# Performance work log

Measured on AMD Instinct MI355X. Metric: run time of the kernel, lower is better.

## Reference

```python
import jax, jax.numpy as jnp
import numpy as np

K = 1024       # vq_codebook_size
DC = 64        # vq_code_dim
BETA = 0.25    # commitment cost
DECAY = 0.99   # EMA decay
EPS = 1e-05


def setup_inputs() -> dict:
    key = jax.random.key(0)
    k1, k2, k3 = jax.random.split(key, 3)
    B, H, W = 32, 64, 64
    return {
        "z_e": jax.random.normal(k1, (B, DC, H, W), dtype=jnp.float32),
        "embedding": jax.random.normal(k2, (K, DC), dtype=jnp.float32),
        "cluster_size": jnp.ones((K,), dtype=jnp.float32),
        "embed_avg": jax.random.normal(k3, (K, DC), dtype=jnp.float32),
    }


def reference(z_e, embedding, cluster_size, embed_avg):
    B, D, H, W = z_e.shape
    # flat: [N, D] detached codes, N = B*H*W
    flat = jax.lax.stop_gradient(z_e).transpose(0, 2, 3, 1).reshape(-1, D).astype(jnp.float32)
    distances = ((flat ** 2).sum(1, keepdims=True)
                 + (embedding ** 2).sum(1)
                 - 2.0 * flat @ embedding.T)
    indices = jnp.argmin(distances, axis=-1)          # [N]
    z_q_flat = embedding[indices]                      # gather [N, D]

    # EMA statistics (training path): one-hot sums via segment_sum (scatter-add)
    counts = jax.ops.segment_sum(jnp.ones_like(indices, dtype=jnp.float32), indices, num_segments=K)
    dw = jax.ops.segment_sum(flat, indices, num_segments=K)  # encodings.T @ flat
    new_cluster_size = cluster_size * DECAY + (1.0 - DECAY) * counts
    new_embed_avg = embed_avg * DECAY + (1.0 - DECAY) * dw
    n = new_cluster_size.sum()
    smoothed = (new_cluster_size + EPS) / (n + K * EPS) * n
    new_embedding = new_embed_avg / smoothed[:, None]

    z_q = z_q_flat.reshape(B, H, W, D).transpose(0, 3, 1, 2)  # [B, D, H, W]
    commitment_loss = BETA * jnp.mean((z_e.astype(jnp.float32) - jax.lax.stop_gradient(z_q)) ** 2)
    # straight-through estimator
    z_q_st = z_e + jax.lax.stop_gradient(z_q.astype(z_e.dtype) - z_e)
    return (z_q_st, indices.reshape(B, H, W), commitment_loss,
            new_embedding, new_cluster_size, new_embed_avg)
```

## Files before the change

kernel.cpp:

```cpp
#include <hip/hip_runtime.h>

#define KCB   1024
#define DCV   64
#define HWN   4096
#define CHW   262144
#define NTOT  131072

#define O_ZQ   0
#define O_IDX  8388608
#define O_LOSS 8519680
#define O_NE   8519681
#define O_NCS  8585217
#define O_NEA  8586241

#define W_LOSS  0
#define W_CTR   64
#define W_E2    256
#define W_SM    4352
#define W_HIT   8448
#define W_LOT   139520
#define W_EMBT  270592
#define W_RLIST 532736

#define RCAP   65536
#define MARGIN 0.015f

typedef __attribute__((ext_vector_type(8))) short short8v;
typedef __attribute__((ext_vector_type(4))) float f32x4;

__device__ __forceinline__ unsigned short rne16(float f) {
    unsigned u = __float_as_uint(f);
    unsigned r = (u + 0x7FFFu + ((u >> 16) & 1u)) >> 16;
    return (unsigned short)r;
}

__global__ __launch_bounds__(256) void k_init(
    const float* __restrict__ emb, const float* __restrict__ ea,
    const float* __restrict__ cs, float* __restrict__ out,
    float* __restrict__ e2, short* __restrict__ hiT, short* __restrict__ loT,
    float* __restrict__ embT, double* __restrict__ loss, int* __restrict__ ctr)
{
    int j = blockIdx.x * 256 + threadIdx.x;
    out[O_NEA + j] = 0.99f * ea[j];

    {
        int code = j >> 6, d = j & 63;
        embT[d * KCB + code] = emb[j];
    }
    if (j < KCB) {
        out[O_NCS + j] = 0.99f * cs[j];
        const float* er = emb + j * DCV;
        float s = 0.f;
        #pragma unroll
        for (int d = 0; d < DCV; ++d) { float v = er[d]; s = fmaf(v, v, s); }
        e2[j] = s;
    }
    if (j < 8192) {
        int code = j >> 3, q = j & 7;
        const float* src = emb + code * DCV + q * 8;
        short8v h, l;
        #pragma unroll
        for (int t = 0; t < 8; ++t) {
            float x = src[t];
            unsigned short hb = rne16(x);
            float xh = __uint_as_float(((unsigned)hb) << 16);
            h[t] = (short)hb;
            l[t] = (short)rne16(x - xh);
        }
        *(short8v*)(hiT + (size_t)(q * KCB + code) * 8) = h;
        *(short8v*)(loT + (size_t)(q * KCB + code) * 8) = l;
    }
    if (j == 0) { *loss = 0.0; *ctr = 0; }
}

__global__ __launch_bounds__(256, 4) void k_dist(
    const float* __restrict__ ze, const short* __restrict__ hiT,
    const short* __restrict__ loT, const float* __restrict__ e2g,
    float* __restrict__ out, int* __restrict__ ctr, int* __restrict__ rlist)
{
    __shared__ short ldsH[8 * 128 * 8];
    __shared__ short ldsL[8 * 128 * 8];
    __shared__ float e2s[KCB];

    int tid  = threadIdx.x;
    int lane = tid & 63, w = tid >> 6;
    int g = lane >> 4, c = lane & 15;

    for (int i = tid; i < KCB; i += 256) e2s[i] = e2g[i];

    int rowbase = blockIdx.x * 128 + w * 32;
    short8v ahi[2][2], alo[2][2];
    #pragma unroll
    for (int t = 0; t < 2; ++t) {
        int n = rowbase + t * 16 + c;
        const float* base = ze + (size_t)(n >> 12) * CHW + (n & 4095);
        #pragma unroll
        for (int kh = 0; kh < 2; ++kh) {
            #pragma unroll
            for (int j = 0; j < 8; ++j) {
                int k = kh * 32 + g * 8 + j;
                float x = base[(size_t)k * HWN];
                unsigned short hb = rne16(x);
                float xh = __uint_as_float(((unsigned)hb) << 16);
                ahi[t][kh][j] = (short)hb;
                alo[t][kh][j] = (short)rne16(x - xh);
            }
        }
    }

    float best[8], second[8];
    int   bidx[8];
    #pragma unroll
    for (int i = 0; i < 8; ++i) { best[i] = 3.4e38f; second[i] = 3.4e38f; bidx[i] = 0; }

    for (int ch = 0; ch < 8; ++ch) {
        __syncthreads();
        #pragma unroll
        for (int r = 0; r < 8; ++r) {
            int u = r * 256 + tid;
            int arr = u >> 10;
            int rest = u & 1023;
            int q = rest >> 7, lc = rest & 127;
            const short* s = (arr ? loT : hiT) + (size_t)(q * KCB + ch * 128 + lc) * 8;
            short* d = (arr ? ldsL : ldsH) + rest * 8;
            *(short8v*)d = *(const short8v*)s;
        }
        __syncthreads();

        #pragma unroll 1
        for (int sub = 0; sub < 8; ++sub) {
            int boff = (sub * 16 + c) * 8;
            short8v bh0 = *(const short8v*)&ldsH[(g * 128) * 8 + boff];
            short8v bh1 = *(const short8v*)&ldsH[((4 + g) * 128) * 8 + boff];
            short8v bl0 = *(const short8v*)&ldsL[(g * 128) * 8 + boff];
            short8v bl1 = *(const short8v*)&ldsL[((4 + g) * 128) * 8 + boff];

            f32x4 a0 = {0.f, 0.f, 0.f, 0.f}, a1 = {0.f, 0.f, 0.f, 0.f};
            a0 = __builtin_amdgcn_mfma_f32_16x16x32_bf16(ahi[0][0], bh0, a0, 0, 0, 0);
            a1 = __builtin_amdgcn_mfma_f32_16x16x32_bf16(ahi[1][0], bh0, a1, 0, 0, 0);
            a0 = __builtin_amdgcn_mfma_f32_16x16x32_bf16(ahi[0][1], bh1, a0, 0, 0, 0);
            a1 = __builtin_amdgcn_mfma_f32_16x16x32_bf16(ahi[1][1], bh1, a1, 0, 0, 0);
            a0 = __builtin_amdgcn_mfma_f32_16x16x32_bf16(ahi[0][0], bl0, a0, 0, 0, 0);
            a1 = __builtin_amdgcn_mfma_f32_16x16x32_bf16(ahi[1][0], bl0, a1, 0, 0, 0);
            a0 = __builtin_amdgcn_mfma_f32_16x16x32_bf16(ahi[0][1], bl1, a0, 0, 0, 0);
            a1 = __builtin_amdgcn_mfma_f32_16x16x32_bf16(ahi[1][1], bl1, a1, 0, 0, 0);
            a0 = __builtin_amdgcn_mfma_f32_16x16x32_bf16(alo[0][0], bh0, a0, 0, 0, 0);
            a1 = __builtin_amdgcn_mfma_f32_16x16x32_bf16(alo[1][0], bh0, a1, 0, 0, 0);
            a0 = __builtin_amdgcn_mfma_f32_16x16x32_bf16(alo[0][1], bh1, a0, 0, 0, 0);
            a1 = __builtin_amdgcn_mfma_f32_16x16x32_bf16(alo[1][1], bh1, a1, 0, 0, 0);

            float e2v = e2s[ch * 128 + sub * 16 + c];
            int  code = ch * 128 + sub * 16 + c;
            #pragma unroll
            for (int t = 0; t < 2; ++t) {
                f32x4 av = t ? a1 : a0;
                #pragma unroll
                for (int r = 0; r < 4; ++r) {
                    int i = t * 4 + r;
                    float s = fmaf(-2.f, av[r], e2v);
                    bool lb = s < best[i];
                    float m = lb ? best[i] : s;
                    second[i] = fminf(second[i], m);
                    best[i]   = fminf(best[i], s);
                    bidx[i]   = lb ? code : bidx[i];
                }
            }
        }
    }

    #pragma unroll
    for (int i = 0; i < 8; ++i) {
        float b = best[i], s2 = second[i];
        int bi = bidx[i];
        #pragma unroll
        for (int m = 1; m < 16; m <<= 1) {
            float ob = __shfl_xor(b, m, 64);
            float os = __shfl_xor(s2, m, 64);
            int   oi = __shfl_xor(bi, m, 64);
            float ns = fminf(fmaxf(b, ob), fminf(s2, os));
            bi = (ob < b || (ob == b && oi < bi)) ? oi : bi;
            b  = fminf(b, ob);
            s2 = ns;
        }
        if (c == 0) {
            int t = i >> 2, r = i & 3;
            int n = rowbase + t * 16 + g * 4 + r;
            out[O_IDX + n] = (float)bi;
            if (s2 - b < MARGIN) {
                int p = atomicAdd(ctr, 1);
                if (p < RCAP) rlist[p] = n;
            }
        }
    }
}

__global__ __launch_bounds__(256) void k_refine(
    const float* __restrict__ ze, const float* __restrict__ emb,
    float* __restrict__ out, const int* __restrict__ ctr,
    const int* __restrict__ rlist)
{
    int lane = threadIdx.x & 63;
    int gw   = (blockIdx.x * blockDim.x + threadIdx.x) >> 6;
    int nw   = (gridDim.x * blockDim.x) >> 6;
    int cnt  = *ctr;
    if (cnt > RCAP) cnt = RCAP;

    for (int i = gw; i < cnt; i += nw) {
        int n = rlist[i];
        const float* zp = ze + (size_t)(n >> 12) * CHW + (n & 4095);
        float x[DCV];
        #pragma unroll
        for (int d = 0; d < DCV; ++d) x[d] = zp[(size_t)d * HWN];

        double bd = 1e300;
        int    bi = 0;
        #pragma unroll 1
        for (int cc = 0; cc < KCB / 64; ++cc) {
            int k = cc * 64 + lane;
            const float4* eb4 = (const float4*)(emb + k * DCV);
            double a0 = 0.0, a1 = 0.0;
            #pragma unroll
            for (int q = 0; q < DCV / 4; ++q) {
                float4 v = eb4[q];
                double d0 = (double)x[q * 4 + 0] - (double)v.x;
                double d1 = (double)x[q * 4 + 1] - (double)v.y;
                double d2 = (double)x[q * 4 + 2] - (double)v.z;
                double d3 = (double)x[q * 4 + 3] - (double)v.w;
                a0 = fma(d0, d0, a0); a1 = fma(d1, d1, a1);
                a0 = fma(d2, d2, a0); a1 = fma(d3, d3, a1);
            }
            double dist = a0 + a1;
            if (dist < bd || (dist == bd && k < bi)) { bd = dist; bi = k; }
        }
        #pragma unroll
        for (int off = 32; off > 0; off >>= 1) {
            double od = __shfl_xor(bd, off, 64);
            int    oi = __shfl_xor(bi, off, 64);
            if (od < bd || (od == bd && oi < bi)) { bd = od; bi = oi; }
        }
        if (lane == 0) out[O_IDX + n] = (float)bi;
    }
}

__global__ __launch_bounds__(256) void k_final(
    const float* __restrict__ ze, const float* __restrict__ embT,
    float* __restrict__ out, double* __restrict__ loss)
{
    int blk = blockIdx.x;
    int b   = blk >> 4;
    int hw  = (blk & 15) * 256 + threadIdx.x;
    int n   = b * HWN + hw;

    int myidx = (int)out[O_IDX + n];

    const float* zp = ze  + (size_t)b * CHW + hw;
    float*       zq = out + O_ZQ + (size_t)b * CHW + hw;

    float lp = 0.f;
    #pragma unroll 8
    for (int d = 0; d < DCV; ++d) {
        float x = zp[(size_t)d * HWN];
        float e = embT[d * KCB + myidx];
        float df = x - e;
        lp = fmaf(df, df, lp);
        zq[(size_t)d * HWN] = x + (e - x);
    }

    #pragma unroll
    for (int off = 32; off > 0; off >>= 1) lp += __shfl_down(lp, off, 64);

    __shared__ float wsum[4];
    int lane = threadIdx.x & 63, wid = threadIdx.x >> 6;
    if (lane == 0) wsum[wid] = lp;
    __syncthreads();
    if (threadIdx.x == 0) {
        double s = (double)wsum[0] + wsum[1] + wsum[2] + wsum[3];
        atomicAdd(loss, s);
    }
}

__global__ __launch_bounds__(256) void k_dw_part(
    const float* __restrict__ ze, const float* __restrict__ outIdx,
    float* __restrict__ out)
{
    int gidx = blockIdx.x >> 5, b = blockIdx.x & 31;
    __shared__ float acc[8 * KCB];
    __shared__ float cnt[KCB];
    for (int i = threadIdx.x; i < 8 * KCB; i += 256) acc[i] = 0.f;
    if (gidx == 0) for (int i = threadIdx.x; i < KCB; i += 256) cnt[i] = 0.f;
    __syncthreads();

    const float* zp  = ze + (size_t)b * CHW + (size_t)gidx * 8 * HWN;
    const float* ipf = outIdx + b * HWN;
    for (int hw = threadIdx.x; hw < HWN; hw += 256) {
        int idx = (int)ipf[hw];
        #pragma unroll
        for (int i = 0; i < 8; ++i) atomicAdd(&acc[idx * 8 + i], zp[(size_t)i * HWN + hw]);
        if (gidx == 0) atomicAdd(&cnt[idx], 1.f);
    }
    __syncthreads();

    for (int j = threadIdx.x; j < 8192; j += 256) {
        float v = acc[j];
        if (v != 0.f) atomicAdd(&out[O_NEA + (j >> 3) * DCV + gidx * 8 + (j & 7)], 0.01f * v);
    }
    if (gidx == 0)
        for (int k = threadIdx.x; k < KCB; k += 256) {
            float cv = cnt[k];
            if (cv != 0.f) atomicAdd(&out[O_NCS + k], 0.01f * cv);
        }
}

__global__ __launch_bounds__(1024) void k_stats(
    float* __restrict__ out, float* __restrict__ sm,
    const double* __restrict__ loss)
{
    int k = threadIdx.x;
    float ncs = out[O_NCS + k];
    __shared__ float red[KCB];
    red[k] = ncs;
    __syncthreads();
    for (int s = 512; s > 0; s >>= 1) {
        if (k < s) red[k] += red[k + s];
        __syncthreads();
    }
    float n = red[0];
    sm[k] = (ncs + 1e-5f) / (n + (float)KCB * 1e-5f) * n;
    if (k == 0) out[O_LOSS] = (float)(0.25 * (*loss) / (double)(NTOT * DCV));
}

__global__ __launch_bounds__(256) void k_embed(
    float* __restrict__ out, const float* __restrict__ sm)
{
    int j = blockIdx.x * 256 + threadIdx.x;
    out[O_NE + j] = out[O_NEA + j] / sm[j >> 6];
}

extern "C" void kernel_launch(void* const* d_in, const int* in_sizes, int n_in,
                              void* d_out, int out_size, void* d_ws, size_t ws_size,
                              hipStream_t stream)
{
    const float* ze  = (const float*)d_in[0];
    const float* emb = (const float*)d_in[1];
    const float* cs  = (const float*)d_in[2];
    const float* ea  = (const float*)d_in[3];
    float* out = (float*)d_out;

    char*   w     = (char*)d_ws;
    double* loss  = (double*)(w + W_LOSS);
    int*    ctr   = (int*)(w + W_CTR);
    float*  e2    = (float*)(w + W_E2);
    float*  sm    = (float*)(w + W_SM);
    short*  hiT   = (short*)(w + W_HIT);
    short*  loT   = (short*)(w + W_LOT);
    float*  embT  = (float*)(w + W_EMBT);
    int*    rlist = (int*)(w + W_RLIST);

    k_init   <<<256, 256, 0, stream>>>(emb, ea, cs, out, e2, hiT, loT, embT, loss, ctr);
    k_dist   <<<1024, 256, 0, stream>>>(ze, hiT, loT, e2, out, ctr, rlist);
    k_refine <<<256, 256, 0, stream>>>(ze, emb, out, ctr, rlist);
    k_final  <<<512, 256, 0, stream>>>(ze, embT, out, loss);
    k_dw_part<<<256, 256, 0, stream>>>(ze, (const float*)(out + O_IDX), out);
    k_stats  <<<1, 1024, 0, stream>>>(out, sm, loss);
    k_embed  <<<256, 256, 0, stream>>>(out, sm);
}
```

Before: 268.9 us.

## Fuse z_q/loss pass with dw scatter, merge stats into embed, tune dist

Merges the straight-through/commitment-loss pass into the per-batch dw/count scatter kernel so z_e and the indices are read once, and folds the cluster-size reduction and embedding normalisation into a single kernel. Seven launches become five. It also lowers the refine margin for ambiguous argmin candidates and relaxes the occupancy hint on the distance kernel. The fused kernel runs only 256 blocks, fewer than the separate 512-block z_q pass, which may lower memory parallelism. The smaller margin risks missing near-tie rows that need exact refinement.

```diff
diff --git a/kernel.cpp b/kernel.cpp
--- a/kernel.cpp
+++ b/kernel.cpp
@@ -16,14 +16,13 @@
 #define W_LOSS  0
 #define W_CTR   64
 #define W_E2    256
-#define W_SM    4352
 #define W_HIT   8448
 #define W_LOT   139520
 #define W_EMBT  270592
 #define W_RLIST 532736
 
 #define RCAP   65536
-#define MARGIN 0.015f
+#define MARGIN 0.01f
 
 typedef __attribute__((ext_vector_type(8))) short short8v;
 typedef __attribute__((ext_vector_type(4))) float f32x4;
@@ -73,7 +72,7 @@
     if (j == 0) { *loss = 0.0; *ctr = 0; }
 }
 
-__global__ __launch_bounds__(256, 4) void k_dist(
+__global__ __launch_bounds__(256, 2) void k_dist(
     const float* __restrict__ ze, const short* __restrict__ hiT,
     const short* __restrict__ loT, const float* __restrict__ e2g,
     float* __restrict__ out, int* __restrict__ ctr, int* __restrict__ rlist)
@@ -242,34 +241,40 @@
     }
 }
 
-__global__ __launch_bounds__(256) void k_final(
+__global__ __launch_bounds__(256) void k_post(
     const float* __restrict__ ze, const float* __restrict__ embT,
     float* __restrict__ out, double* __restrict__ loss)
 {
-    int blk = blockIdx.x;
-    int b   = blk >> 4;
-    int hw  = (blk & 15) * 256 + threadIdx.x;
-    int n   = b * HWN + hw;
-
-    int myidx = (int)out[O_IDX + n];
-
-    const float* zp = ze  + (size_t)b * CHW + hw;
-    float*       zq = out + O_ZQ + (size_t)b * CHW + hw;
+    int gidx = blockIdx.x >> 5, b = blockIdx.x & 31;
+    __shared__ float acc[8 * KCB];
+    __shared__ float cnt[KCB];
+    __shared__ float wsum[4];
+    for (int i = threadIdx.x; i < 8 * KCB; i += 256) acc[i] = 0.f;
+    if (gidx == 0) for (int i = threadIdx.x; i < KCB; i += 256) cnt[i] = 0.f;
+    __syncthreads();
+
+    const float* zp  = ze  + (size_t)b * CHW + (size_t)gidx * 8 * HWN;
+    float*       zq  = out + O_ZQ + (size_t)b * CHW + (size_t)gidx * 8 * HWN;
+    const float* ipf = out + O_IDX + b * HWN;
+    const float* eT  = embT + (size_t)gidx * 8 * KCB;
 
     float lp = 0.f;
-    #pragma unroll 8
-    for (int d = 0; d < DCV; ++d) {
-        float x = zp[(size_t)d * HWN];
-        float e = embT[d * KCB + myidx];
-        float df = x - e;
-        lp = fmaf(df, df, lp);
-        zq[(size_t)d * HWN] = x + (e - x);
+    for (int hw = threadIdx.x; hw < HWN; hw += 256) {
+        int idx = (int)ipf[hw];
+        #pragma unroll
+        for (int i = 0; i < 8; ++i) {
+            float x = zp[(size_t)i * HWN + hw];
+            float e = eT[i * KCB + idx];
+            float df = x - e;
+            lp = fmaf(df, df, lp);
+            zq[(size_t)i * HWN + hw] = x + (e - x);
+            atomicAdd(&acc[idx * 8 + i], x);
+        }
+        if (gidx == 0) atomicAdd(&cnt[idx], 1.f);
     }
 
     #pragma unroll
     for (int off = 32; off > 0; off >>= 1) lp += __shfl_down(lp, off, 64);
-
-    __shared__ float wsum[4];
     int lane = threadIdx.x & 63, wid = threadIdx.x >> 6;
     if (lane == 0) wsum[wid] = lp;
     __syncthreads();
@@ -277,28 +282,6 @@
         double s = (double)wsum[0] + wsum[1] + wsum[2] + wsum[3];
         atomicAdd(loss, s);
     }
-}
-
-__global__ __launch_bounds__(256) void k_dw_part(
-    const float* __restrict__ ze, const float* __restrict__ outIdx,
-    float* __restrict__ out)
-{
-    int gidx = blockIdx.x >> 5, b = blockIdx.x & 31;
-    __shared__ float acc[8 * KCB];
-    __shared__ float cnt[KCB];
-    for (int i = threadIdx.x; i < 8 * KCB; i += 256) acc[i] = 0.f;
-    if (gidx == 0) for (int i = threadIdx.x; i < KCB; i += 256) cnt[i] = 0.f;
-    __syncthreads();
-
-    const float* zp  = ze + (size_t)b * CHW + (size_t)gidx * 8 * HWN;
-    const float* ipf = outIdx + b * HWN;
-    for (int hw = threadIdx.x; hw < HWN; hw += 256) {
-        int idx = (int)ipf[hw];
-        #pragma unroll
-        for (int i = 0; i < 8; ++i) atomicAdd(&acc[idx * 8 + i], zp[(size_t)i * HWN + hw]);
-        if (gidx == 0) atomicAdd(&cnt[idx], 1.f);
-    }
-    __syncthreads();
 
     for (int j = threadIdx.x; j < 8192; j += 256) {
         float v = acc[j];
@@ -311,29 +294,29 @@
         }
 }
 
-__global__ __launch_bounds__(1024) void k_stats(
-    float* __restrict__ out, float* __restrict__ sm,
-    const double* __restrict__ loss)
-{
-    int k = threadIdx.x;
+__global__ __launch_bounds__(256) void k_fin(
+    float* __restrict__ out, const double* __restrict__ loss)
+{
+    __shared__ float red[4];
+    int t = threadIdx.x;
+    float s = 0.f;
+    #pragma unroll
+    for (int q = 0; q < 4; ++q) s += out[O_NCS + t * 4 + q];
+    #pragma unroll
+    for (int off = 32; off > 0; off >>= 1) s += __shfl_down(s, off, 64);
+    int lane = t & 63, wid = t >> 6;
+    if (lane == 0) red[wid] = s;
+    __syncthreads();
+    float n = red[0] + red[1] + red[2] + red[3];
+
+    int j = blockIdx.x * 256 + t;
+    int k = j >> 6;
     float ncs = out[O_NCS + k];
-    __shared__ float red[KCB];
-    red[k] = ncs;
-    __syncthreads();
-    for (int s = 512; s > 0; s >>= 1) {
-        if (k < s) red[k] += red[k + s];
-        __syncthreads();
-    }
-    float n = red[0];
-    sm[k] = (ncs + 1e-5f) / (n + (float)KCB * 1e-5f) * n;
-    if (k == 0) out[O_LOSS] = (float)(0.25 * (*loss) / (double)(NTOT * DCV));
-}
-
-__global__ __launch_bounds__(256) void k_embed(
-    float* __restrict__ out, const float* __restrict__ sm)
-{
-    int j = blockIdx.x * 256 + threadIdx.x;
-    out[O_NE + j] = out[O_NEA + j] / sm[j >> 6];
+    float sm = (ncs + 1e-5f) / (n + (float)KCB * 1e-5f) * n;
+    out[O_NE + j] = out[O_NEA + j] / sm;
+
+    if (blockIdx.x == 0 && t == 0)
+        out[O_LOSS] = (float)(0.25 * (*loss) / (double)(NTOT * DCV));
 }
 
 extern "C" void kernel_launch(void* const* d_in, const int* in_sizes, int n_in,
@@ -350,17 +333,14 @@
     double* loss  = (double*)(w + W_LOSS);
     int*    ctr   = (int*)(w + W_CTR);
     float*  e2    = (float*)(w + W_E2);
-    float*  sm    = (float*)(w + W_SM);
     short*  hiT   = (short*)(w + W_HIT);
     short*  loT   = (short*)(w + W_LOT);
     float*  embT  = (float*)(w + W_EMBT);
     int*    rlist = (int*)(w + W_RLIST);
 
-    k_init   <<<256, 256, 0, stream>>>(emb, ea, cs, out, e2, hiT, loT, embT, loss, ctr);
-    k_dist   <<<1024, 256, 0, stream>>>(ze, hiT, loT, e2, out, ctr, rlist);
-    k_refine <<<256, 256, 0, stream>>>(ze, emb, out, ctr, rlist);
-    k_final  <<<512, 256, 0, stream>>>(ze, embT, out, loss);
-    k_dw_part<<<256, 256, 0, stream>>>(ze, (const float*)(out + O_IDX), out);
-    k_stats  <<<1, 1024, 0, stream>>>(out, sm, loss);
-    k_embed  <<<256, 256, 0, stream>>>(out, sm);
-}
+    k_init  <<<256, 256, 0, stream>>>(emb, ea, cs, out, e2, hiT, loT, embT, loss, ctr);
+    k_dist  <<<1024, 256, 0, stream>>>(ze, hiT, loT, e2, out, ctr, rlist);
+    k_refine<<<256, 256, 0, stream>>>(ze, emb, out, ctr, rlist);
+    k_post  <<<256, 256, 0, stream>>>(ze, embT, out, loss);
+    k_fin   <<<256, 256, 0, stream>>>(out, loss);
+}
```

Result: faster. 247.6 us (-7.9%).
